# Optimization experiments

Hardware: AMD Instinct MI355X
Metric: run time of the kernel (lower is better)

Reference implementation:

```python
import jax, jax.numpy as jnp
import numpy as np


def setup_inputs() -> dict:
    key = jax.random.key(0)
    kq, kk, kv = jax.random.split(key, 3)
    B, Lq, Lk, D = 4, 4096, 4096, 64
    return {
        "Q": jax.random.normal(kq, (B, Lq, D), dtype=jnp.float32),
        "K": jax.random.normal(kk, (B, Lk, D), dtype=jnp.float32),
        "V": jax.random.normal(kv, (B, Lk, D), dtype=jnp.float32),
    }


def reference(Q, K, V):
    # scores: [B, Lq, Lk]  (no 1/sqrt(d) scaling in the original module)
    scores = jnp.einsum("bqd,bkd->bqk", Q, K)
    attn = jax.nn.softmax(scores, axis=-1)
    # output: [B, Lq, D]
    return jnp.einsum("bqk,bkd->bqd", attn, V)
```

## Files before the change

kernel.cpp:

```cpp
#include <hip/hip_runtime.h>
#include <cmath>


#define B_    4
#define LQ    4096
#define LK    4096
#define DH    64
#define BQ    256
#define NQT3  (B_ * LQ / BQ)
#define NKVT  (LK / 128)
#define NROWS (B_ * LQ)
#define LOG2E 1.44269504088896f
#define C0    63.4785817991f

typedef _Float16 f16x8 __attribute__((ext_vector_type(8)));
typedef _Float16 f16x4 __attribute__((ext_vector_type(4)));
typedef float    f32x4 __attribute__((ext_vector_type(4)));
typedef short    s16x8 __attribute__((ext_vector_type(8)));
typedef int      i32x4 __attribute__((ext_vector_type(4)));

__device__ inline float exp2_(float x) {
#if __has_builtin(__builtin_amdgcn_exp2f)
  return __builtin_amdgcn_exp2f(x);
#else
  return exp2f(x);
#endif
}

__device__ inline unsigned pkbf16(float lo, float hi) {
  return __builtin_amdgcn_perm(__float_as_uint(hi), __float_as_uint(lo),
                               0x07060302u);
}

__device__ inline unsigned short bf16rne(float f) {
  unsigned u = __float_as_uint(f);
  return (unsigned short)((u + 0x7FFF + ((u >> 16) & 1)) >> 16);
}

__device__ inline void async16(const void* g, void* l) {
  __builtin_amdgcn_global_load_lds(
      (const __attribute__((address_space(1))) unsigned int*)g,
      (__attribute__((address_space(3))) unsigned int*)l, 16, 0, 0);
}

__global__ __launch_bounds__(256) void convert_kv8(
    const float* __restrict__ K, const float* __restrict__ V,
    const float* __restrict__ Q, _Float16* __restrict__ Kh,
    unsigned short* __restrict__ Vb, _Float16* __restrict__ Qh) {
  __shared__ unsigned short Vs[64 * 68];
  const int tid = threadIdx.x;
  const int bb = blockIdx.x;

  if (bb < 256) {
    const int b = bb >> 6, tile = (bb >> 1) & 31, half = bb & 1;
    const int kv0 = tile * 128 + half * 64;
    for (int i = 0; i < 2; ++i) {
      int q = i * 256 + tid;
      int r = q >> 3, g = q & 7;
      const float* src = K + ((size_t)(b * LK + kv0 + r)) * DH + g * 8;
      float4 a = *(const float4*)src;
      float4 d = *(const float4*)(src + 4);
      f16x8 hv = {(_Float16)(a.x * LOG2E), (_Float16)(a.y * LOG2E),
                  (_Float16)(a.z * LOG2E), (_Float16)(a.w * LOG2E),
                  (_Float16)(d.x * LOG2E), (_Float16)(d.y * LOG2E),
                  (_Float16)(d.z * LOG2E), (_Float16)(d.w * LOG2E)};
      int gp = g ^ (r & 7);
      size_t dst = ((size_t)(b * 32 + tile) * 128 + half * 64 + r) * 64 + gp * 8;
      *(f16x8*)(&Kh[dst]) = hv;
    }
  } else if (bb < 512) {
    const int cc = bb - 256;
    const int b = cc >> 6, tile = (cc >> 1) & 31, half = cc & 1;
    const int kv0 = tile * 128 + half * 64;
    for (int i = 0; i < 4; ++i) {
      int idx = i * 256 + tid;
      int vr = idx >> 4, c4 = idx & 15;
      float4 v = *(const float4*)(&V[((size_t)(b * LK + kv0 + vr)) * DH + c4 * 4]);
      Vs[vr * 68 + c4 * 4 + 0] = bf16rne(v.x);
      Vs[vr * 68 + c4 * 4 + 1] = bf16rne(v.y);
      Vs[vr * 68 + c4 * 4 + 2] = bf16rne(v.z);
      Vs[vr * 68 + c4 * 4 + 3] = bf16rne(v.w);
    }
    __syncthreads();
    for (int i = 0; i < 2; ++i) {
      int q = i * 256 + tid;
      int d = q >> 3, gl = q & 7;
      int g = half * 8 + gl;
      unsigned short ov[8];
#pragma unroll
      for (int j = 0; j < 8; ++j) {
        int p = g * 8 + j;
        int c = p >> 5, w5 = p & 31;
        int qd = w5 >> 3, jj = w5 & 7, hh = jj >> 2, r = jj & 3;
        int sL = 32 * c + 16 * hh + 4 * qd + r - 64 * half;
        ov[j] = Vs[sL * 68 + d];
      }
      int gp = g ^ (d & 7);
      size_t dst = ((size_t)(b * 32 + tile) * 64 + d) * 128 + gp * 8;
      s16x8 o8;
#pragma unroll
      for (int j = 0; j < 8; ++j) o8[j] = (short)ov[j];
      *(s16x8*)(&Vb[dst]) = o8;
    }
  } else {
    const int u = bb - 512;
    for (int i = 0; i < 4; ++i) {
      int idx = i * 256 + tid;
      int r = idx >> 4, c4 = idx & 15;
      size_t off = ((size_t)u * 64 + r) * DH + c4 * 4;
      float4 v = *(const float4*)(&Q[off]);
      f16x4 h = {(_Float16)v.x, (_Float16)v.y, (_Float16)v.z, (_Float16)v.w};
      *(f16x4*)(&Qh[off]) = h;
    }
  }
}

__global__ __launch_bounds__(256, 2) void ca_flash9(
    const _Float16* __restrict__ Qh, const _Float16* __restrict__ Kh,
    const unsigned short* __restrict__ Vb, float* __restrict__ Out,
    _Float16* __restrict__ Opart, float* __restrict__ Lw, int nsplit) {
  __shared__ _Float16 KsH[128 * 64];
  __shared__ unsigned short VtH[64 * 128];

  const int tid  = threadIdx.x;
  const int wave = tid >> 6;
  const int lane = tid & 63;
  const int quad = lane >> 4;
  const int l16  = lane & 15;
  const int e    = quad ^ (l16 & 7);

  const int qt    = blockIdx.x;
  const int b     = qt >> 4;
  const int qbase = (qt & 15) * BQ;
  const int sp    = blockIdx.y;
  const int t0 = (NKVT * sp) / nsplit;
  const int t1 = (NKVT * (sp + 1)) / nsplit;

  f16x8 qf[4][2];
#pragma unroll
  for (int sub = 0; sub < 4; ++sub) {
    int qrow = qbase + wave * 64 + sub * 16 + l16;
    const _Float16* qp = Qh + ((size_t)b * LQ + qrow) * DH + quad * 8;
#pragma unroll
    for (int kk = 0; kk < 2; ++kk)
      qf[sub][kk] = *(const f16x8*)(qp + kk * 32);
  }

  f32x4 o[4][5];
#pragma unroll
  for (int sub = 0; sub < 4; ++sub)
#pragma unroll
    for (int td = 0; td < 5; ++td) o[sub][td] = (f32x4){0.f, 0.f, 0.f, 0.f};

  s16x8 ones;
#pragma unroll
  for (int j = 0; j < 8; ++j) ones[j] = (short)0x3F80;

  const char* kg = (const char*)Kh + ((size_t)(b * 32 + t0)) * 16384;
  const char* vg = (const char*)Vb + ((size_t)(b * 32 + t0)) * 16384;
  char* ksB = (char*)KsH;
  char* vtB = (char*)VtH;
  const char* kR = ksB + l16 * 128;
  const char* vR = vtB + l16 * 256;

  for (int tile = t0; tile < t1; ++tile) {
    __syncthreads();
    const char* sg = (wave < 2) ? (kg + wave * 8192) : (vg + (wave - 2) * 8192);
    char*       sd = (wave < 2) ? (ksB + wave * 8192) : (vtB + (wave - 2) * 8192);
#pragma unroll
    for (int i = 0; i < 8; ++i) async16(sg + i * 1024 + lane * 16, sd + i * 1024);
    __syncthreads();
    kg += 16384; vg += 16384;

#pragma unroll
    for (int c = 0; c < 4; ++c) {
      f32x4 sv[4][2];
#pragma unroll
      for (int sub = 0; sub < 4; ++sub)
#pragma unroll
        for (int tt = 0; tt < 2; ++tt)
          sv[sub][tt] = (f32x4){-C0, -C0, -C0, -C0};
#pragma unroll
      for (int kk = 0; kk < 2; ++kk) {
        int ko = (e ^ (4 * kk)) * 16;
#pragma unroll
        for (int tt = 0; tt < 2; ++tt) {
          f16x8 bk = *(const f16x8*)(kR + (2 * c + tt) * 2048 + ko);
#pragma unroll
          for (int sub = 0; sub < 4; ++sub)
            sv[sub][tt] = __builtin_amdgcn_mfma_f32_16x16x32_f16(
                bk, qf[sub][kk], sv[sub][tt], 0, 0, 0);
        }
      }

      s16x8 ap[4];
#pragma unroll
      for (int sub = 0; sub < 4; ++sub) {
        unsigned u0 = pkbf16(exp2_(sv[sub][0][0]), exp2_(sv[sub][0][1]));
        unsigned u1 = pkbf16(exp2_(sv[sub][0][2]), exp2_(sv[sub][0][3]));
        unsigned u2 = pkbf16(exp2_(sv[sub][1][0]), exp2_(sv[sub][1][1]));
        unsigned u3 = pkbf16(exp2_(sv[sub][1][2]), exp2_(sv[sub][1][3]));
        i32x4 iv = {(int)u0, (int)u1, (int)u2, (int)u3};
        ap[sub] = __builtin_bit_cast(s16x8, iv);
      }

      int vo = (e ^ (4 * c)) * 16;
#pragma unroll
      for (int td = 0; td < 4; ++td) {
        s16x8 bv = *(const s16x8*)(vR + td * 4096 + vo);
#pragma unroll
        for (int sub = 0; sub < 4; ++sub)
          o[sub][td] = __builtin_amdgcn_mfma_f32_16x16x32_bf16(
              ap[sub], bv, o[sub][td], 0, 0, 0);
      }
#pragma unroll
      for (int sub = 0; sub < 4; ++sub)
        o[sub][4] = __builtin_amdgcn_mfma_f32_16x16x32_bf16(
            ap[sub], ones, o[sub][4], 0, 0, 0);
    }
  }

  if (nsplit == 1) {
#pragma unroll
    for (int sub = 0; sub < 4; ++sub)
#pragma unroll
      for (int r = 0; r < 4; ++r) {
        float inv = 1.0f / (o[sub][4][r] + 1e-35f);
        size_t row = (size_t)b * LQ + qbase + wave * 64 + sub * 16 + quad * 4 + r;
#pragma unroll
        for (int td = 0; td < 4; ++td)
          Out[row * DH + td * 16 + l16] = o[sub][td][r] * inv;
      }
    return;
  }

#pragma unroll
  for (int sub = 0; sub < 4; ++sub)
#pragma unroll
    for (int r = 0; r < 4; ++r) {
      float l = o[sub][4][r];
      float inv = 1.0f / (l + 1e-35f);
      size_t g = (size_t)qt * BQ + wave * 64 + sub * 16 + quad * 4 + r;
      size_t prow = (size_t)sp * NROWS + g;
#pragma unroll
      for (int td = 0; td < 4; ++td)
        Opart[prow * DH + td * 16 + l16] = (_Float16)(o[sub][td][r] * inv);
      if (l16 == 0) Lw[prow] = l;
    }
}

__global__ __launch_bounds__(256) void ca_combine9(
    const _Float16* __restrict__ Opart, const float* __restrict__ Lw,
    float* __restrict__ Out, int nsplit) {
  const int idx = blockIdx.x * 256 + threadIdx.x;
  const int g = idx >> 4;
  const int c0 = (idx & 15) * 4;
  float den = 1e-30f;
  float a0 = 0.f, a1 = 0.f, a2 = 0.f, a3 = 0.f;
  for (int s = 0; s < nsplit; ++s) {
    size_t prow = (size_t)s * NROWS + g;
    float w = Lw[prow];
    f16x4 v = *(const f16x4*)(&Opart[prow * DH + c0]);
    a0 += w * (float)v[0]; a1 += w * (float)v[1];
    a2 += w * (float)v[2]; a3 += w * (float)v[3];
    den += w;
  }
  float inv = 1.0f / den;
  float4 ov = {a0 * inv, a1 * inv, a2 * inv, a3 * inv};
  *(float4*)(&Out[(size_t)g * DH + c0]) = ov;
}

#define LDSS 72
__global__ __launch_bounds__(256) void ca_flash_naive(
    const float* __restrict__ Q, const float* __restrict__ K,
    const float* __restrict__ V, float* __restrict__ Out) {
  __shared__ _Float16 Qs[64 * LDSS];
  __shared__ _Float16 Ks[64 * LDSS];
  __shared__ _Float16 Vt[64 * LDSS];
  __shared__ _Float16 Ps[64 * LDSS];
  const int tid = threadIdx.x, wave = tid >> 6, lane = tid & 63;
  const int quad = lane >> 4, l16 = lane & 15;
  const int b = blockIdx.x >> 6, qbase = (blockIdx.x & 63) * 64;
  for (int i = 0; i < 4; ++i) {
    int idx = (i * 256 + tid) * 4;
    int r = idx >> 6, c = idx & 63;
    float4 q4 = *(const float4*)(&Q[((size_t)b * LQ + qbase + r) * DH + c]);
    f16x4 hh = {(_Float16)q4.x, (_Float16)q4.y, (_Float16)q4.z, (_Float16)q4.w};
    *(f16x4*)(&Qs[r * LDSS + c]) = hh;
  }
  __syncthreads();
  f16x8 qf[2];
  qf[0] = *(const f16x8*)(&Qs[(wave * 16 + l16) * LDSS + quad * 8]);
  qf[1] = *(const f16x8*)(&Qs[(wave * 16 + l16) * LDSS + quad * 8 + 32]);
  float m_i[4], l_i[4];
  f32x4 o[4];
  for (int r = 0; r < 4; ++r) {
    m_i[r] = -INFINITY; l_i[r] = 0.f; o[r] = (f32x4){0.f, 0.f, 0.f, 0.f};
  }
  for (int kv0 = 0; kv0 < LK; kv0 += 64) {
    __syncthreads();
    for (int i = 0; i < 4; ++i) {
      int idx = (i * 256 + tid) * 4;
      int r = idx >> 6, c = idx & 63;
      float4 k4 = *(const float4*)(&K[((size_t)b * LK + kv0 + r) * DH + c]);
      f16x4 hh = {(_Float16)k4.x, (_Float16)k4.y, (_Float16)k4.z, (_Float16)k4.w};
      *(f16x4*)(&Ks[r * LDSS + c]) = hh;
      float4 v4 = *(const float4*)(&V[((size_t)b * LK + kv0 + r) * DH + c]);
      Vt[(c + 0) * LDSS + r] = (_Float16)v4.x;
      Vt[(c + 1) * LDSS + r] = (_Float16)v4.y;
      Vt[(c + 2) * LDSS + r] = (_Float16)v4.z;
      Vt[(c + 3) * LDSS + r] = (_Float16)v4.w;
    }
    __syncthreads();
    f32x4 sv[4];
    for (int t = 0; t < 4; ++t) sv[t] = (f32x4){0.f, 0.f, 0.f, 0.f};
    for (int kk = 0; kk < 2; ++kk)
      for (int t = 0; t < 4; ++t) {
        f16x8 bk = *(const f16x8*)(&Ks[(t * 16 + l16) * LDSS + quad * 8 + kk * 32]);
        sv[t] = __builtin_amdgcn_mfma_f32_16x16x32_f16(qf[kk], bk, sv[t], 0, 0, 0);
      }
    for (int r = 0; r < 4; ++r) {
      float mx = fmaxf(fmaxf(sv[0][r], sv[1][r]), fmaxf(sv[2][r], sv[3][r]));
      for (int off = 1; off < 16; off <<= 1) mx = fmaxf(mx, __shfl_xor(mx, off, 64));
      float mnew = fmaxf(m_i[r], mx);
      float alpha = __expf(m_i[r] - mnew);
      float rs = 0.f;
      for (int t = 0; t < 4; ++t) { float p = __expf(sv[t][r] - mnew); sv[t][r] = p; rs += p; }
      for (int off = 1; off < 16; off <<= 1) rs += __shfl_xor(rs, off, 64);
      l_i[r] = l_i[r] * alpha + rs;
      m_i[r] = mnew;
      for (int td = 0; td < 4; ++td) o[td][r] *= alpha;
    }
    for (int t = 0; t < 4; ++t)
      for (int r = 0; r < 4; ++r)
        Ps[(wave * 16 + quad * 4 + r) * LDSS + t * 16 + l16] = (_Float16)sv[t][r];
    for (int kk = 0; kk < 2; ++kk) {
      f16x8 ap = *(const f16x8*)(&Ps[(wave * 16 + l16) * LDSS + quad * 8 + kk * 32]);
      for (int td = 0; td < 4; ++td) {
        f16x8 bv = *(const f16x8*)(&Vt[(td * 16 + l16) * LDSS + quad * 8 + kk * 32]);
        o[td] = __builtin_amdgcn_mfma_f32_16x16x32_f16(ap, bv, o[td], 0, 0, 0);
      }
    }
  }
  float inv_l[4];
  for (int r = 0; r < 4; ++r) inv_l[r] = 1.0f / l_i[r];
  for (int td = 0; td < 4; ++td)
    for (int r = 0; r < 4; ++r) {
      size_t row = (size_t)b * LQ + qbase + wave * 16 + quad * 4 + r;
      Out[row * DH + td * 16 + l16] = o[td][r] * inv_l[r];
    }
}

extern "C" void kernel_launch(void* const* d_in, const int* in_sizes, int n_in,
                              void* d_out, int out_size, void* d_ws, size_t ws_size,
                              hipStream_t stream) {
  const float* Q = (const float*)d_in[0];
  const float* K = (const float*)d_in[1];
  const float* V = (const float*)d_in[2];
  float* Out = (float*)d_out;

  const size_t sKh = (size_t)B_ * LK * DH * sizeof(_Float16);
  const size_t sVb = (size_t)B_ * LK * DH * sizeof(unsigned short);
  const size_t sQh = (size_t)NROWS * DH * sizeof(_Float16);
  const size_t base = sKh + sVb + sQh;
  auto opSize = [](int sp) { return (size_t)sp * NROWS * DH * sizeof(_Float16); };
  auto lwSize = [](int sp) { return (size_t)sp * NROWS * sizeof(float); };

  int split = 0;
  if (base + opSize(8) + lwSize(8) <= ws_size) split = 8;
  else if (base + opSize(4) + lwSize(4) <= ws_size) split = 4;
  else if (base + opSize(2) + lwSize(2) <= ws_size) split = 2;
  else if (base <= ws_size) split = 1;

  char* ws = (char*)d_ws;
  if (split >= 1) {
    _Float16* Kh = (_Float16*)ws;
    unsigned short* Vb = (unsigned short*)(ws + sKh);
    _Float16* Qh = (_Float16*)(ws + sKh + sVb);
    convert_kv8<<<dim3(768), dim3(256), 0, stream>>>(K, V, Q, Kh, Vb, Qh);
    if (split == 1) {
      ca_flash9<<<dim3(NQT3, 1), dim3(256), 0, stream>>>(
          Qh, Kh, Vb, Out, nullptr, nullptr, 1);
    } else {
      _Float16* Op = (_Float16*)(ws + base);
      float* Lwp = (float*)(ws + base + opSize(split));
      ca_flash9<<<dim3(NQT3, split), dim3(256), 0, stream>>>(
          Qh, Kh, Vb, Out, Op, Lwp, split);
      ca_combine9<<<dim3(NROWS * DH / 4 / 256), dim3(256), 0, stream>>>(
          Op, Lwp, Out, split);
    }
  } else {
    ca_flash_naive<<<dim3(256), dim3(256), 0, stream>>>(Q, K, V, Out);
  }
}
```

Baseline: 95.08 us.

## Double-buffer K/V tiles in LDS to overlap async loads with MFMA compute

Shared-memory K and V tiles become two buffers. The next tile is loaded asynchronously while the current one is being computed, which replaces the two barriers per tile with a single barrier at the end of each iteration. The goal is to hide global-to-LDS load latency behind the score and PV MFMA work. In exchange, each block uses twice the LDS (64KB), which may limit how many blocks fit per CU. The overlap is also modest because each split covers only a few tiles.

```diff
diff --git a/kernel.cpp b/kernel.cpp
--- a/kernel.cpp
+++ b/kernel.cpp
@@ -115,12 +115,12 @@
   }
 }
 
-__global__ __launch_bounds__(256, 2) void ca_flash9(
+__global__ __launch_bounds__(256, 2) void ca_flash11(
     const _Float16* __restrict__ Qh, const _Float16* __restrict__ Kh,
     const unsigned short* __restrict__ Vb, float* __restrict__ Out,
     _Float16* __restrict__ Opart, float* __restrict__ Lw, int nsplit) {
-  __shared__ _Float16 KsH[128 * 64];
-  __shared__ unsigned short VtH[64 * 128];
+  __shared__ _Float16 KsH[2][128 * 64];
+  __shared__ unsigned short VtH[2][64 * 128];
 
   const int tid  = threadIdx.x;
   const int wave = tid >> 6;
@@ -160,17 +160,31 @@
   const char* vg = (const char*)Vb + ((size_t)(b * 32 + t0)) * 16384;
   char* ksB = (char*)KsH;
   char* vtB = (char*)VtH;
-  const char* kR = ksB + l16 * 128;
-  const char* vR = vtB + l16 * 256;
-
-  for (int tile = t0; tile < t1; ++tile) {
-    __syncthreads();
+
+  {
     const char* sg = (wave < 2) ? (kg + wave * 8192) : (vg + (wave - 2) * 8192);
     char*       sd = (wave < 2) ? (ksB + wave * 8192) : (vtB + (wave - 2) * 8192);
 #pragma unroll
     for (int i = 0; i < 8; ++i) async16(sg + i * 1024 + lane * 16, sd + i * 1024);
-    __syncthreads();
     kg += 16384; vg += 16384;
+  }
+  __syncthreads();
+
+  for (int tile = t0; tile < t1; ++tile) {
+    const int buf = (tile - t0) & 1;
+    if (tile + 1 < t1) {
+      const int bn = buf ^ 1;
+      const char* sg = (wave < 2) ? (kg + wave * 8192) : (vg + (wave - 2) * 8192);
+      char*       sd = (wave < 2) ? (ksB + bn * 16384 + wave * 8192)
+                                  : (vtB + bn * 16384 + (wave - 2) * 8192);
+#pragma unroll
+      for (int i = 0; i < 8; ++i)
+        async16(sg + i * 1024 + lane * 16, sd + i * 1024);
+      kg += 16384; vg += 16384;
+    }
+
+    const char* kR = ksB + buf * 16384 + l16 * 128;
+    const char* vR = vtB + buf * 16384 + l16 * 256;
 
 #pragma unroll
     for (int c = 0; c < 4; ++c) {
@@ -218,6 +232,8 @@
         o[sub][4] = __builtin_amdgcn_mfma_f32_16x16x32_bf16(
             ap[sub], ones, o[sub][4], 0, 0, 0);
     }
+
+    __syncthreads();
   }
 
   if (nsplit == 1) {
@@ -249,7 +265,7 @@
     }
 }
 
-__global__ __launch_bounds__(256) void ca_combine9(
+__global__ __launch_bounds__(256) void ca_combine11(
     const _Float16* __restrict__ Opart, const float* __restrict__ Lw,
     float* __restrict__ Out, int nsplit) {
   const int idx = blockIdx.x * 256 + threadIdx.x;
@@ -379,14 +395,14 @@
     _Float16* Qh = (_Float16*)(ws + sKh + sVb);
     convert_kv8<<<dim3(768), dim3(256), 0, stream>>>(K, V, Q, Kh, Vb, Qh);
     if (split == 1) {
-      ca_flash9<<<dim3(NQT3, 1), dim3(256), 0, stream>>>(
+      ca_flash11<<<dim3(NQT3, 1), dim3(256), 0, stream>>>(
           Qh, Kh, Vb, Out, nullptr, nullptr, 1);
     } else {
       _Float16* Op = (_Float16*)(ws + base);
       float* Lwp = (float*)(ws + base + opSize(split));
-      ca_flash9<<<dim3(NQT3, split), dim3(256), 0, stream>>>(
+      ca_flash11<<<dim3(NQT3, split), dim3(256), 0, stream>>>(
           Qh, Kh, Vb, Out, Op, Lwp, split);
-      ca_combine9<<<dim3(NROWS * DH / 4 / 256), dim3(256), 0, stream>>>(
+      ca_combine11<<<dim3(NROWS * DH / 4 / 256), dim3(256), 0, stream>>>(
           Op, Lwp, Out, split);
     }
   } else {
```

After: 95.22 us. Within noise of the previous version (+0.2%).
